# Performance work log

Measured on AMD Instinct MI355X. Metric: run time of the kernel, lower is better.

Reference implementation:

```python
import jax, jax.numpy as jnp
import numpy as np

EMBED = 512
HEADS = 8
EPS = 1e-5


def setup_inputs() -> dict:
    key = jax.random.key(0)
    ks = jax.random.split(key, 8)
    B, Sq, Skv, D = 4, 2048, 2048, EMBED
    return {
        "layer_input": jax.random.normal(ks[0], (B, Sq, D), jnp.float32),
        "cross_attn_input": jax.random.normal(ks[1], (B, Skv, D), jnp.float32),
        "Wq": jax.random.normal(ks[2], (D, D), jnp.float32) * (D ** -0.5),
        "bq": jnp.zeros((D,), jnp.float32),
        "Wkv": jax.random.normal(ks[3], (D, 2 * D), jnp.float32) * (D ** -0.5),
        "bkv": jnp.zeros((2 * D,), jnp.float32),
        "Wo": jax.random.normal(ks[4], (D, D), jnp.float32) * (D ** -0.5),
        "bo": jnp.zeros((D,), jnp.float32),
        "gamma": jnp.ones((D,), jnp.float32),
        "beta": jnp.zeros((D,), jnp.float32),
    }


def _split_heads(x):
    # ... s (h d) -> ... h s d
    *lead, s, hd = x.shape
    d = hd // HEADS
    return jnp.moveaxis(x.reshape(*lead, s, HEADS, d), -2, -3)


def _merge_heads(x):
    # ... h s d -> ... s (h d)
    x = jnp.moveaxis(x, -3, -2)
    *lead, s, h, d = x.shape
    return x.reshape(*lead, s, h * d)


def reference(layer_input, cross_attn_input, Wq, bq, Wkv, bkv, Wo, bo, gamma, beta):
    scale = (EMBED // HEADS) ** -0.5
    res = layer_input
    q = layer_input @ Wq + bq
    kv = cross_attn_input @ Wkv + bkv
    k, v = jnp.split(kv, 2, axis=-1)
    q, k, v = map(_split_heads, (q, k, v))  # [B, H, S, d]
    scores = jnp.einsum('bhqc,bhkc->bhqk', q, k) * scale
    weights = jax.nn.softmax(scores, axis=-1)  # dropout p=0 -> identity
    out = jnp.einsum('bhqk,bhkc->bhqc', weights, v)
    out = _merge_heads(out)
    out = out @ Wo + bo
    x = out + res
    mu = jnp.mean(x, axis=-1, keepdims=True)
    var = jnp.mean(jnp.square(x - mu), axis=-1, keepdims=True)
    return (x - mu) * jax.lax.rsqrt(var + EPS) * gamma + beta
```

## Files before the change

kernel.cpp:

```cpp
#include <hip/hip_runtime.h>
#include <hip/hip_bf16.h>
#include <stdint.h>

#define SEQ    2048
#define DM     512
#define NHEAD  8
#define HD     64
#define BATCH  4
#define MTOT   (BATCH*SEQ)

typedef __attribute__((ext_vector_type(4))) float  f32x4;
typedef __attribute__((ext_vector_type(8))) short  bf16x8;
typedef __attribute__((ext_vector_type(8))) unsigned short u16x8;
typedef __attribute__((ext_vector_type(4))) unsigned short u16x4;
typedef __attribute__((ext_vector_type(4))) float  fl4;
typedef __attribute__((ext_vector_type(2))) unsigned u32x2;
typedef __attribute__((ext_vector_type(4))) unsigned u32x4;

__device__ __forceinline__ unsigned short f2bf(float f) {
  union { float f; unsigned u; } c; c.f = f;
  return (unsigned short)((c.u + 0x7fffu + ((c.u >> 16) & 1u)) >> 16);
}

__device__ __forceinline__ float bf2f(unsigned short s) {
  unsigned u = (unsigned)s << 16;
  float f; __builtin_memcpy(&f, &u, 4);
  return f;
}

__device__ __forceinline__ void load_lds16(const void* g, void* l) {
  __builtin_amdgcn_global_load_lds((__attribute__((address_space(1))) void*)g,
                                   (__attribute__((address_space(3))) void*)l,
                                   16, 0, 0);
}

__device__ __forceinline__ u32x2 ds_tr16(const void* p) {
  u32x2 r;
  asm volatile("ds_read_b64_tr_b16 %0, %1"
               : "=v"(r)
               : "v"((__attribute__((address_space(3))) const void*)p));
  return r;
}

__device__ __forceinline__ unsigned pack_bf2(float lo, float hi) {
  __hip_bfloat162 h2 = __float22bfloat162_rn(float2{lo, hi});
  unsigned u; __builtin_memcpy(&u, &h2, 4);
  return u;
}

__global__ void k_pre(const float* __restrict__ X, unsigned short* __restrict__ Xb,
                      const float* __restrict__ C, unsigned short* __restrict__ Cb,
                      const float* __restrict__ Wq, unsigned short* __restrict__ Wqt,
                      const float* __restrict__ Wkv, unsigned short* __restrict__ Wkvt,
                      const float* __restrict__ Wo, unsigned short* __restrict__ Wot) {
  __shared__ __align__(16) unsigned short t[64][66];
  int bid = blockIdx.x, tid = threadIdx.x;
  if (bid < 8192) {
    const float* src = (bid < 4096) ? X : C;
    unsigned short* dst = (bid < 4096) ? Xb : Cb;
    int i = (bid & 4095) * 256 + tid;
    fl4 v = *(const fl4*)(src + (size_t)i * 4);
    u32x2 o;
    o[0] = pack_bf2(v[0], v[1]);
    o[1] = pack_bf2(v[2], v[3]);
    *(u32x2*)((void*)(dst + (size_t)i * 4)) = o;
    return;
  }
  int tjob = bid - 8192;
  const float* W; unsigned short* Wt; int Nd, bx, by;
  if (tjob < 64)       { W = Wq;  Wt = Wqt;  Nd = 512;  bx = tjob & 7;  by = tjob >> 3; }
  else if (tjob < 192) { int u = tjob - 64;  W = Wkv; Wt = Wkvt; Nd = 1024; bx = u & 15; by = u >> 4; }
  else                 { int u = tjob - 192; W = Wo;  Wt = Wot;  Nd = 512;  bx = u & 7;  by = u >> 3; }
  int k0 = by * 64, n0 = bx * 64;
  int r = tid >> 2, cs = (tid & 3) * 16;
  const float* src = W + (size_t)(k0 + r) * Nd + n0 + cs;
#pragma unroll
  for (int i = 0; i < 4; ++i) {
    fl4 v = *(const fl4*)(src + i * 4);
    *(unsigned*)&t[r][cs + i*4]     = pack_bf2(v[0], v[1]);
    *(unsigned*)&t[r][cs + i*4 + 2] = pack_bf2(v[2], v[3]);
  }
  __syncthreads();
  unsigned short* drow = Wt + (size_t)(n0 + r) * 512 + k0 + cs;
#pragma unroll
  for (int half = 0; half < 2; ++half) {
    u16x8 o;
#pragma unroll
    for (int i = 0; i < 8; ++i) o[i] = t[cs + half*8 + i][r];
    *(u16x8*)(drow + half * 8) = o;
  }
}

template<int RESID>
__device__ __forceinline__ void gemm128x64(
    const unsigned short* __restrict__ A,
    const unsigned short* __restrict__ Bt,
    const float* __restrict__ bias,
    const unsigned short* __restrict__ res,
    unsigned short* __restrict__ Cout,
    int N, int K, int m0, int n0, float osc,
    unsigned short* Als, unsigned short* Bls) {
  int tid  = threadIdx.x;
  int lane = tid & 63, wave = tid >> 6;
  int q = lane & 15, lk = lane >> 4;
  f32x4 acc[2][4];
#pragma unroll
  for (int mt = 0; mt < 2; ++mt)
#pragma unroll
    for (int nt = 0; nt < 4; ++nt) acc[mt][nt] = f32x4{0.f,0.f,0.f,0.f};

  const unsigned short* gA[4];
#pragma unroll
  for (int it = 0; it < 4; ++it) {
    int idx = tid + it * 256;
    int row = idx >> 3, ch = idx & 7, sc = ch ^ (row & 7);
    gA[it] = A + (size_t)(m0 + row) * K + sc * 8;
  }
  const unsigned short* gB[2];
#pragma unroll
  for (int it = 0; it < 2; ++it) {
    int idx = tid + it * 256;
    int row = idx >> 3, ch = idx & 7, sc = ch ^ (row & 7);
    gB[it] = Bt + (size_t)(n0 + row) * K + sc * 8;
  }
  char* aD = (char*)Als + tid * 16;
  char* bD = (char*)Bls + tid * 16;

#pragma unroll
  for (int it = 0; it < 4; ++it) { load_lds16(gA[it], aD + it * 4096); gA[it] += 64; }
#pragma unroll
  for (int it = 0; it < 2; ++it) { load_lds16(gB[it], bD + it * 4096); gB[it] += 64; }
  __syncthreads();

  int nkb = K >> 6;
  int buf = 0;
  for (int kb = 0; kb < nkb; ++kb) {
    if (kb + 1 < nkb) {
      char* aN = aD + (buf ^ 1) * 16384;
      char* bN = bD + (buf ^ 1) * 8192;
#pragma unroll
      for (int it = 0; it < 4; ++it) { load_lds16(gA[it], aN + it * 4096); gA[it] += 64; }
#pragma unroll
      for (int it = 0; it < 2; ++it) { load_lds16(gB[it], bN + it * 4096); gB[it] += 64; }
    }
    const char* aR = (const char*)Als + buf * 16384;
    const char* bR = (const char*)Bls + buf * 8192;
#pragma unroll
    for (int ks = 0; ks < 2; ++ks) {
      bf16x8 a[2], b[4];
#pragma unroll
      for (int mt = 0; mt < 2; ++mt) {
        int row = wave * 32 + mt * 16 + q;
        a[mt] = *(const bf16x8*)(aR + row * 128 + (((ks*4 + lk) ^ (row & 7)) * 16));
      }
#pragma unroll
      for (int nt = 0; nt < 4; ++nt) {
        int row = nt * 16 + q;
        b[nt] = *(const bf16x8*)(bR + row * 128 + (((ks*4 + lk) ^ (row & 7)) * 16));
      }
#pragma unroll
      for (int mt = 0; mt < 2; ++mt)
#pragma unroll
        for (int nt = 0; nt < 4; ++nt)
          acc[mt][nt] = __builtin_amdgcn_mfma_f32_16x16x32_bf16(a[mt], b[nt], acc[mt][nt], 0, 0, 0);
    }
    __syncthreads();
    buf ^= 1;
  }
#pragma unroll
  for (int nt = 0; nt < 4; ++nt) {
    int col = n0 + nt * 16 + q;
    float bv = bias[col];
#pragma unroll
    for (int mt = 0; mt < 2; ++mt) {
      int rowb = m0 + wave * 32 + mt * 16 + lk * 4;
#pragma unroll
      for (int rr = 0; rr < 4; ++rr) {
        float v = acc[mt][nt][rr] + bv;
        size_t off = (size_t)(rowb + rr) * N + col;
        if (RESID) Cout[off] = f2bf(v + bf2f(res[off]));
        else       Cout[off] = f2bf(v * osc);
      }
    }
  }
}

__global__ __launch_bounds__(256, 3)
void k_projmm(const unsigned short* __restrict__ Xb, const unsigned short* __restrict__ Cb,
              const unsigned short* __restrict__ Wqt, const unsigned short* __restrict__ Wkvt,
              const float* __restrict__ bq, const float* __restrict__ bkv,
              unsigned short* __restrict__ Qb, unsigned short* __restrict__ KVb) {
  __shared__ __align__(16) unsigned short Als[2 * 128 * 64];
  __shared__ __align__(16) unsigned short Bls[2 * 64 * 64];
  int bid = blockIdx.x;
  int l = (bid & 7) * 192 + (bid >> 3);
  const float c1 = 0.125f * 1.44269504088896340736f;
  if (l < 512) {
    int m = l >> 3, n = l & 7;
    gemm128x64<0>(Xb, Wqt, bq, nullptr, Qb, 512, 512, m * 128, n * 64, c1, Als, Bls);
  } else {
    int l2 = l - 512;
    int m = l2 >> 4, n = l2 & 15;
    gemm128x64<0>(Cb, Wkvt, bkv, nullptr, KVb, 1024, 512, m * 128, n * 64, 1.0f, Als, Bls);
  }
}

__global__ __launch_bounds__(256, 3)
void k_omm(const unsigned short* __restrict__ Abuf, const unsigned short* __restrict__ Wot,
           const float* __restrict__ bo, const unsigned short* __restrict__ residb,
           unsigned short* __restrict__ tmp) {
  __shared__ __align__(16) unsigned short Als[2 * 128 * 64];
  __shared__ __align__(16) unsigned short Bls[2 * 64 * 64];
  int bid = blockIdx.x;
  int l = (bid & 7) * 64 + (bid >> 3);
  int m = l >> 3, n = l & 7;
  gemm128x64<1>(Abuf, Wot, bo, residb, tmp, 512, 512, m * 128, n * 64, 1.0f, Als, Bls);
}

__global__ __launch_bounds__(256, 3)
void k_attn(const unsigned short* __restrict__ Qb,
            const unsigned short* __restrict__ KVb,
            unsigned short* __restrict__ Ab) {
  __shared__ __align__(16) unsigned short Klds[2][64 * 64];
  __shared__ __align__(16) unsigned short Vlds[4][4096];
  int tid  = threadIdx.x;
  int lane = tid & 63, wave = tid >> 6;
  int q    = lane & 15, lk = lane >> 4;
  int bid = blockIdx.x;
  int swz = (bid & 7) * 128 + (bid >> 3);
  int qt = swz & 31, bh = swz >> 5;
  int b  = bh >> 3, h = bh & 7;
  int q0 = qt * 64 + wave * 16;
  const size_t kvbase = (size_t)b * SEQ * 1024;

  bf16x8 qf0, qf1;
  {
    size_t qrow = (size_t)b * SEQ + q0 + q;
    qf0 = *(const bf16x8*)(Qb + qrow * DM + h * HD + lk * 8);
    qf1 = *(const bf16x8*)(Qb + qrow * DM + h * HD + 32 + lk * 8);
  }
  f32x4 acc[4];
#pragma unroll
  for (int i = 0; i < 4; ++i) acc[i] = f32x4{0.f,0.f,0.f,0.f};
  float l = 0.f;
  u32x4 pbA[2];

  const unsigned short *gK0, *gK1, *gV0, *gV1;
  {
    int r0 = tid >> 3, s0_ = (tid & 7) ^ (r0 & 7);
    gK0 = KVb + kvbase + (size_t)r0 * 1024 + h * HD + s0_ * 8;
    int i1 = tid + 256, r1 = i1 >> 3, s1_ = (i1 & 7) ^ (r1 & 7);
    gK1 = KVb + kvbase + (size_t)r1 * 1024 + h * HD + s1_ * 8;
    int dt0 = tid >> 7, w0 = tid & 127, p0 = w0 >> 1, c80 = (w0 & 1) * 8;
    int t0 = (p0 & 32) + (((p0 >> 2) & 3) << 3) + (((p0 >> 4) & 1) << 2) + (p0 & 3);
    gV0 = KVb + kvbase + (size_t)t0 * 1024 + 512 + h * HD + dt0 * 16 + c80;
    int i1v = tid + 256, dt1 = i1v >> 7, w1 = i1v & 127, p1 = w1 >> 1, c81 = (w1 & 1) * 8;
    int t1 = (p1 & 32) + (((p1 >> 2) & 3) << 3) + (((p1 >> 4) & 1) << 2) + (p1 & 3);
    gV1 = KVb + kvbase + (size_t)t1 * 1024 + 512 + h * HD + dt1 * 16 + c81;
  }
  char* kw0 = (char*)Klds[0] + tid * 16;
  char* kw1 = (char*)Klds[1] + tid * 16;
  char* vw0 = (char*)Vlds[0] + tid * 16;
  char* vw1 = (char*)Vlds[1] + tid * 16;
  char* vw2 = (char*)Vlds[2] + tid * 16;
  char* vw3 = (char*)Vlds[3] + tid * 16;
  const char* kr0 = (const char*)Klds[0];
  const char* kr1 = (const char*)Klds[1];
  const char* vr0 = (const char*)Vlds[0] + lane * 8;
  const char* vr1 = (const char*)Vlds[1] + lane * 8;
  const char* vr2 = (const char*)Vlds[2] + lane * 8;
  const char* vr3 = (const char*)Vlds[3] + lane * 8;

#define STAGE(kd_, vd_) do {                        \
    load_lds16(gK0, (kd_));                         \
    load_lds16(gK1, (kd_) + 4096);                  \
    load_lds16(gV0, (vd_));                         \
    load_lds16(gV1, (vd_) + 4096);                  \
    gK0 += 65536; gK1 += 65536;                     \
    gV0 += 65536; gV1 += 65536;                     \
  } while (0)

#define ABODY(DO_PV, DO_STAGE, kdst_, vdst_, krd_, vprd_) do {               \
    if (DO_STAGE) STAGE(kdst_, vdst_);                                       \
    if (DO_PV) {                                                             \
      u32x2 tr[4][2][2];                                                     \
      _Pragma("unroll")                                                      \
      for (int dt = 0; dt < 4; ++dt)                                         \
        _Pragma("unroll")                                                    \
        for (int ks2 = 0; ks2 < 2; ++ks2)                                    \
          _Pragma("unroll")                                                  \
          for (int u = 0; u < 2; ++u)                                        \
            tr[dt][ks2][u] = ds_tr16((vprd_) + dt * 2048 + ks2 * 1024 + u * 512); \
      asm volatile("s_waitcnt lgkmcnt(0)" ::: "memory");                     \
      __builtin_amdgcn_sched_barrier(0);                                     \
      __builtin_amdgcn_s_setprio(1);                                         \
      _Pragma("unroll")                                                      \
      for (int ks2 = 0; ks2 < 2; ++ks2) {                                    \
        union { u32x4 u; bf16x8 v; } pb;                                     \
        pb.u = pbA[ks2];                                                     \
        _Pragma("unroll")                                                    \
        for (int dt = 0; dt < 4; ++dt) {                                     \
          union { u32x4 u; bf16x8 v; } cv;                                   \
          cv.u[0] = tr[dt][ks2][0][0]; cv.u[1] = tr[dt][ks2][0][1];          \
          cv.u[2] = tr[dt][ks2][1][0]; cv.u[3] = tr[dt][ks2][1][1];          \
          acc[dt] = __builtin_amdgcn_mfma_f32_16x16x32_bf16(cv.v, pb.v, acc[dt], 0, 0, 0); \
        }                                                                    \
      }                                                                      \
      __builtin_amdgcn_s_setprio(0);                                         \
    }                                                                        \
    f32x4 st[4];                                                             \
    _Pragma("unroll")                                                        \
    for (int kt = 0; kt < 4; ++kt) st[kt] = f32x4{0.f,0.f,0.f,0.f};          \
    __builtin_amdgcn_s_setprio(1);                                           \
    _Pragma("unroll")                                                        \
    for (int kt = 0; kt < 4; ++kt) {                                         \
      int row = kt * 16 + q;                                                 \
      bf16x8 kf0 = *(const bf16x8*)((krd_) + row * 128 + ((lk ^ (row & 7)) * 16)); \
      bf16x8 kf1 = *(const bf16x8*)((krd_) + row * 128 + (((4 + lk) ^ (row & 7)) * 16)); \
      st[kt] = __builtin_amdgcn_mfma_f32_16x16x32_bf16(kf0, qf0, st[kt], 0, 0, 0); \
      st[kt] = __builtin_amdgcn_mfma_f32_16x16x32_bf16(kf1, qf1, st[kt], 0, 0, 0); \
    }                                                                        \
    __builtin_amdgcn_s_setprio(0);                                           \
    float p[4][4];                                                           \
    _Pragma("unroll")                                                        \
    for (int kt = 0; kt < 4; ++kt)                                           \
      _Pragma("unroll")                                                      \
      for (int r = 0; r < 4; ++r) {                                          \
        float pe = __builtin_amdgcn_exp2f(st[kt][r]);                        \
        p[kt][r] = pe;                                                       \
        l += pe;                                                             \
      }                                                                      \
    _Pragma("unroll")                                                        \
    for (int ks2 = 0; ks2 < 2; ++ks2) {                                      \
      unsigned u0 = pack_bf2(p[2*ks2][0],     p[2*ks2][1]);                  \
      unsigned u1 = pack_bf2(p[2*ks2][2],     p[2*ks2][3]);                  \
      unsigned u2 = pack_bf2(p[2*ks2 + 1][0], p[2*ks2 + 1][1]);              \
      unsigned u3 = pack_bf2(p[2*ks2 + 1][2], p[2*ks2 + 1][3]);              \
      asm("v_permlane32_swap_b32 %0, %1" : "+v"(u0), "+v"(u2));              \
      asm("v_permlane32_swap_b32 %0, %1" : "+v"(u1), "+v"(u3));              \
      asm("v_permlane16_swap_b32 %0, %1" : "+v"(u0), "+v"(u2));              \
      asm("v_permlane16_swap_b32 %0, %1" : "+v"(u1), "+v"(u3));              \
      pbA[ks2][0] = u0; pbA[ks2][1] = u1;                                    \
      pbA[ks2][2] = u2; pbA[ks2][3] = u3;                                    \
    }                                                                        \
    __syncthreads();                                                         \
  } while (0)

  STAGE(kw0, vw0);
  __syncthreads();

  ABODY(0, 1, kw1, vw1, kr0, vr0);
  ABODY(1, 1, kw0, vw2, kr1, vr0);
  ABODY(1, 1, kw1, vw3, kr0, vr1);
  ABODY(1, 1, kw0, vw0, kr1, vr2);
  for (int g = 0; g < 6; ++g) {
    ABODY(1, 1, kw1, vw1, kr0, vr3);
    ABODY(1, 1, kw0, vw2, kr1, vr0);
    ABODY(1, 1, kw1, vw3, kr0, vr1);
    ABODY(1, 1, kw0, vw0, kr1, vr2);
  }
  ABODY(1, 1, kw1, vw1, kr0, vr3);
  ABODY(1, 1, kw0, vw2, kr1, vr0);
  ABODY(1, 1, kw1, vw3, kr0, vr1);
  ABODY(1, 0, kw0, vw0, kr1, vr2);

  {
    u32x2 tr[4][2][2];
#pragma unroll
    for (int dt = 0; dt < 4; ++dt)
#pragma unroll
      for (int ks2 = 0; ks2 < 2; ++ks2)
#pragma unroll
        for (int u = 0; u < 2; ++u)
          tr[dt][ks2][u] = ds_tr16(vr3 + dt * 2048 + ks2 * 1024 + u * 512);
    asm volatile("s_waitcnt lgkmcnt(0)" ::: "memory");
    __builtin_amdgcn_sched_barrier(0);
#pragma unroll
    for (int ks2 = 0; ks2 < 2; ++ks2) {
      union { u32x4 u; bf16x8 v; } pb;
      pb.u = pbA[ks2];
#pragma unroll
      for (int dt = 0; dt < 4; ++dt) {
        union { u32x4 u; bf16x8 v; } cv;
        cv.u[0] = tr[dt][ks2][0][0]; cv.u[1] = tr[dt][ks2][0][1];
        cv.u[2] = tr[dt][ks2][1][0]; cv.u[3] = tr[dt][ks2][1][1];
        acc[dt] = __builtin_amdgcn_mfma_f32_16x16x32_bf16(cv.v, pb.v, acc[dt], 0, 0, 0);
      }
    }
  }

  l += __shfl_xor(l, 16);
  l += __shfl_xor(l, 32);
  float inv = 1.0f / l;
  size_t orow = ((size_t)b * SEQ + q0 + q) * DM + h * HD + lk * 4;
#pragma unroll
  for (int dt = 0; dt < 4; ++dt) {
    u16x4 o;
#pragma unroll
    for (int r = 0; r < 4; ++r) o[r] = f2bf(acc[dt][r] * inv);
    *(u16x4*)(Ab + orow + dt * 16) = o;
  }
#undef STAGE
#undef ABODY
}

__global__ void k_ln(const unsigned short* __restrict__ x, const float* __restrict__ gamma,
                     const float* __restrict__ beta, float* __restrict__ out) {
  int tid = threadIdx.x, lane = tid & 63, wave = tid >> 6;
  size_t row = (size_t)blockIdx.x * 4 + wave;
  u16x8 xv = *(const u16x8*)(x + row * DM + lane * 8);
  float v[8];
#pragma unroll
  for (int i = 0; i < 8; ++i) v[i] = bf2f(xv[i]);
  float s  = (v[0]+v[1]) + (v[2]+v[3]) + (v[4]+v[5]) + (v[6]+v[7]);
  float ss = (v[0]*v[0]+v[1]*v[1]) + (v[2]*v[2]+v[3]*v[3])
           + (v[4]*v[4]+v[5]*v[5]) + (v[6]*v[6]+v[7]*v[7]);
#pragma unroll
  for (int off = 1; off < 64; off <<= 1) {
    s  += __shfl_xor(s, off);
    ss += __shfl_xor(ss, off);
  }
  float mu  = s * (1.0f / DM);
  float var = ss * (1.0f / DM) - mu * mu;
  float w = rsqrtf(var + 1e-5f);
  fl4 g0 = *(const fl4*)(gamma + lane*8), g1 = *(const fl4*)(gamma + lane*8 + 4);
  fl4 b0 = *(const fl4*)(beta + lane*8),  b1 = *(const fl4*)(beta + lane*8 + 4);
  fl4 o0, o1;
#pragma unroll
  for (int i = 0; i < 4; ++i) {
    o0[i] = (v[i]     - mu) * w * g0[i] + b0[i];
    o1[i] = (v[4 + i] - mu) * w * g1[i] + b1[i];
  }
  float* orow = out + row * DM + lane * 8;
  *(fl4*)orow = o0;
  *(fl4*)(orow + 4) = o1;
}

extern "C" void kernel_launch(void* const* d_in, const int* in_sizes, int n_in,
                              void* d_out, int out_size, void* d_ws, size_t ws_size,
                              hipStream_t stream) {
  const float* layer_input = (const float*)d_in[0];
  const float* cross       = (const float*)d_in[1];
  const float* Wq   = (const float*)d_in[2];
  const float* bq   = (const float*)d_in[3];
  const float* Wkv  = (const float*)d_in[4];
  const float* bkv  = (const float*)d_in[5];
  const float* Wo   = (const float*)d_in[6];
  const float* bo   = (const float*)d_in[7];
  const float* gamma = (const float*)d_in[8];
  const float* beta  = (const float*)d_in[9];
  float* out = (float*)d_out;

  char* ws = (char*)d_ws;
  unsigned short* Xb   = (unsigned short*)(ws + (size_t)0);
  unsigned short* Cb   = (unsigned short*)(ws + ((size_t)8  << 20));
  unsigned short* Qb   = (unsigned short*)(ws + ((size_t)16 << 20));
  unsigned short* KVb  = (unsigned short*)(ws + ((size_t)24 << 20));
  unsigned short* Abuf = (unsigned short*)(ws + ((size_t)40 << 20));
  unsigned short* tmpb = (unsigned short*)(ws + ((size_t)48 << 20));
  unsigned short* Wqt  = (unsigned short*)(ws + ((size_t)64 << 20));
  unsigned short* Wkvt = (unsigned short*)(ws + ((size_t)65 << 20));
  unsigned short* Wot  = (unsigned short*)(ws + ((size_t)67 << 20));

  k_pre<<<8448, 256, 0, stream>>>(layer_input, Xb, cross, Cb,
                                  Wq, Wqt, Wkv, Wkvt, Wo, Wot);
  k_projmm<<<1536, 256, 0, stream>>>(Xb, Cb, Wqt, Wkvt, bq, bkv, Qb, KVb);
  k_attn<<<1024, 256, 0, stream>>>(Qb, KVb, Abuf);
  k_omm<<<512, 256, 0, stream>>>(Abuf, Wot, bo, Xb, tmpb);
  k_ln<<<MTOT/4, 256, 0, stream>>>(tmpb, gamma, beta, out);
}
```

Before: 107.2 us.

## Shrink V ring to three buffers, raise attention occupancy, split PV wait

The attention kernel's V staging ring drops from four to three LDS buffers and the launch bound rises from 3 to 4 blocks per CU, cutting shared-memory use so more blocks can be resident. The unrolled K/V schedule is reworked into a 6-step loop that matches the 3-deep V and 2-deep K rotation. The PV transposed loads are reordered so the first k-half's MFMAs can start after a partial lgkmcnt wait, overlapping LDS latency with compute. The tighter register budget risks spills, and the shallower V ring leaves less slack for load latency.

```diff
diff --git a/kernel.cpp b/kernel.cpp
--- a/kernel.cpp
+++ b/kernel.cpp
@@ -217,20 +217,20 @@
   gemm128x64<1>(Abuf, Wot, bo, residb, tmp, 512, 512, m * 128, n * 64, 1.0f, Als, Bls);
 }
 
-__global__ __launch_bounds__(256, 3)
+__global__ __launch_bounds__(256, 4)
 void k_attn(const unsigned short* __restrict__ Qb,
             const unsigned short* __restrict__ KVb,
             unsigned short* __restrict__ Ab) {
   __shared__ __align__(16) unsigned short Klds[2][64 * 64];
-  __shared__ __align__(16) unsigned short Vlds[4][4096];
+  __shared__ __align__(16) unsigned short Vlds[3][4096];
   int tid  = threadIdx.x;
-  int lane = tid & 63, wave = tid >> 6;
+  int lane = tid & 63;
   int q    = lane & 15, lk = lane >> 4;
   int bid = blockIdx.x;
   int swz = (bid & 7) * 128 + (bid >> 3);
   int qt = swz & 31, bh = swz >> 5;
   int b  = bh >> 3, h = bh & 7;
-  int q0 = qt * 64 + wave * 16;
+  int q0 = qt * 64 + (tid >> 6) * 16;
   const size_t kvbase = (size_t)b * SEQ * 1024;
 
   bf16x8 qf0, qf1;
@@ -263,13 +263,11 @@
   char* vw0 = (char*)Vlds[0] + tid * 16;
   char* vw1 = (char*)Vlds[1] + tid * 16;
   char* vw2 = (char*)Vlds[2] + tid * 16;
-  char* vw3 = (char*)Vlds[3] + tid * 16;
   const char* kr0 = (const char*)Klds[0];
   const char* kr1 = (const char*)Klds[1];
   const char* vr0 = (const char*)Vlds[0] + lane * 8;
   const char* vr1 = (const char*)Vlds[1] + lane * 8;
   const char* vr2 = (const char*)Vlds[2] + lane * 8;
-  const char* vr3 = (const char*)Vlds[3] + lane * 8;
 
 #define STAGE(kd_, vd_) do {                        \
     load_lds16(gK0, (kd_));                         \
@@ -283,26 +281,38 @@
 #define ABODY(DO_PV, DO_STAGE, kdst_, vdst_, krd_, vprd_) do {               \
     if (DO_STAGE) STAGE(kdst_, vdst_);                                       \
     if (DO_PV) {                                                             \
-      u32x2 tr[4][2][2];                                                     \
+      u32x2 tr[2][4][2];                                                     \
       _Pragma("unroll")                                                      \
-      for (int dt = 0; dt < 4; ++dt)                                         \
+      for (int ks2 = 0; ks2 < 2; ++ks2)                                      \
         _Pragma("unroll")                                                    \
-        for (int ks2 = 0; ks2 < 2; ++ks2)                                    \
+        for (int dt = 0; dt < 4; ++dt)                                       \
           _Pragma("unroll")                                                  \
           for (int u = 0; u < 2; ++u)                                        \
-            tr[dt][ks2][u] = ds_tr16((vprd_) + dt * 2048 + ks2 * 1024 + u * 512); \
-      asm volatile("s_waitcnt lgkmcnt(0)" ::: "memory");                     \
+            tr[ks2][dt][u] = ds_tr16((vprd_) + dt * 2048 + ks2 * 1024 + u * 512); \
+      asm volatile("s_waitcnt lgkmcnt(8)" ::: "memory");                     \
       __builtin_amdgcn_sched_barrier(0);                                     \
       __builtin_amdgcn_s_setprio(1);                                         \
-      _Pragma("unroll")                                                      \
-      for (int ks2 = 0; ks2 < 2; ++ks2) {                                    \
+      {                                                                      \
         union { u32x4 u; bf16x8 v; } pb;                                     \
-        pb.u = pbA[ks2];                                                     \
+        pb.u = pbA[0];                                                       \
         _Pragma("unroll")                                                    \
         for (int dt = 0; dt < 4; ++dt) {                                     \
           union { u32x4 u; bf16x8 v; } cv;                                   \
-          cv.u[0] = tr[dt][ks2][0][0]; cv.u[1] = tr[dt][ks2][0][1];          \
-          cv.u[2] = tr[dt][ks2][1][0]; cv.u[3] = tr[dt][ks2][1][1];          \
+          cv.u[0] = tr[0][dt][0][0]; cv.u[1] = tr[0][dt][0][1];              \
+          cv.u[2] = tr[0][dt][1][0]; cv.u[3] = tr[0][dt][1][1];              \
+          acc[dt] = __builtin_amdgcn_mfma_f32_16x16x32_bf16(cv.v, pb.v, acc[dt], 0, 0, 0); \
+        }                                                                    \
+      }                                                                      \
+      asm volatile("s_waitcnt lgkmcnt(0)" ::: "memory");                     \
+      __builtin_amdgcn_sched_barrier(0);                                     \
+      {                                                                      \
+        union { u32x4 u; bf16x8 v; } pb;                                     \
+        pb.u = pbA[1];                                                       \
+        _Pragma("unroll")                                                    \
+        for (int dt = 0; dt < 4; ++dt) {                                     \
+          union { u32x4 u; bf16x8 v; } cv;                                   \
+          cv.u[0] = tr[1][dt][0][0]; cv.u[1] = tr[1][dt][0][1];              \
+          cv.u[2] = tr[1][dt][1][0]; cv.u[3] = tr[1][dt][1][1];              \
           acc[dt] = __builtin_amdgcn_mfma_f32_16x16x32_bf16(cv.v, pb.v, acc[dt], 0, 0, 0); \
         }                                                                    \
       }                                                                      \
@@ -350,29 +360,25 @@
   __syncthreads();
 
   ABODY(0, 1, kw1, vw1, kr0, vr0);
-  ABODY(1, 1, kw0, vw2, kr1, vr0);
-  ABODY(1, 1, kw1, vw3, kr0, vr1);
-  ABODY(1, 1, kw0, vw0, kr1, vr2);
-  for (int g = 0; g < 6; ++g) {
-    ABODY(1, 1, kw1, vw1, kr0, vr3);
+  for (int g = 0; g < 5; ++g) {
     ABODY(1, 1, kw0, vw2, kr1, vr0);
-    ABODY(1, 1, kw1, vw3, kr0, vr1);
-    ABODY(1, 1, kw0, vw0, kr1, vr2);
-  }
-  ABODY(1, 1, kw1, vw1, kr0, vr3);
-  ABODY(1, 1, kw0, vw2, kr1, vr0);
-  ABODY(1, 1, kw1, vw3, kr0, vr1);
-  ABODY(1, 0, kw0, vw0, kr1, vr2);
+    ABODY(1, 1, kw1, vw0, kr0, vr1);
+    ABODY(1, 1, kw0, vw1, kr1, vr2);
+    ABODY(1, 1, kw1, vw2, kr0, vr0);
+    ABODY(1, 1, kw0, vw0, kr1, vr1);
+    ABODY(1, 1, kw1, vw1, kr0, vr2);
+  }
+  ABODY(1, 0, kw0, vw0, kr1, vr0);
 
   {
-    u32x2 tr[4][2][2];
-#pragma unroll
-    for (int dt = 0; dt < 4; ++dt)
-#pragma unroll
-      for (int ks2 = 0; ks2 < 2; ++ks2)
+    u32x2 tr[2][4][2];
+#pragma unroll
+    for (int ks2 = 0; ks2 < 2; ++ks2)
+#pragma unroll
+      for (int dt = 0; dt < 4; ++dt)
 #pragma unroll
         for (int u = 0; u < 2; ++u)
-          tr[dt][ks2][u] = ds_tr16(vr3 + dt * 2048 + ks2 * 1024 + u * 512);
+          tr[ks2][dt][u] = ds_tr16(vr1 + dt * 2048 + ks2 * 1024 + u * 512);
     asm volatile("s_waitcnt lgkmcnt(0)" ::: "memory");
     __builtin_amdgcn_sched_barrier(0);
 #pragma unroll
@@ -382,8 +388,8 @@
 #pragma unroll
       for (int dt = 0; dt < 4; ++dt) {
         union { u32x4 u; bf16x8 v; } cv;
-        cv.u[0] = tr[dt][ks2][0][0]; cv.u[1] = tr[dt][ks2][0][1];
-        cv.u[2] = tr[dt][ks2][1][0]; cv.u[3] = tr[dt][ks2][1][1];
+        cv.u[0] = tr[ks2][dt][0][0]; cv.u[1] = tr[ks2][dt][0][1];
+        cv.u[2] = tr[ks2][dt][1][0]; cv.u[3] = tr[ks2][dt][1][1];
         acc[dt] = __builtin_amdgcn_mfma_f32_16x16x32_bf16(cv.v, pb.v, acc[dt], 0, 0, 0);
       }
     }
```

Measured after the change: 107.6 us. About the same (+0.4%).
